# Optimization experiments

Measured on AMD Instinct MI355X. Metric: run time of the kernel, lower is better.

The kernel has to match this reference:

```python
import jax, jax.numpy as jnp
import numpy as np

N_EMBD = 384
HEAD_SIZE = 16

def setup_inputs() -> dict:
    key = jax.random.key(0)
    k1, k2, k3, k4 = jax.random.split(key, 4)
    B, T = 4, 4096
    x = jax.random.normal(k1, (B, T, N_EMBD), dtype=jnp.float32)
    # nn.Linear(n_embd, head_size, bias=False): y = x @ W^T, W: [head_size, n_embd].
    # Store transposed [n_embd, head_size] for direct matmul.
    s = 1.0 / np.sqrt(N_EMBD)
    Wk = jax.random.uniform(k2, (N_EMBD, HEAD_SIZE), jnp.float32, -s, s)
    Wq = jax.random.uniform(k3, (N_EMBD, HEAD_SIZE), jnp.float32, -s, s)
    Wv = jax.random.uniform(k4, (N_EMBD, HEAD_SIZE), jnp.float32, -s, s)
    return {"x": x, "Wk": Wk, "Wq": Wq, "Wv": Wv}

def reference(x, Wk, Wq, Wv):
    B, T, C = x.shape
    k = x @ Wk  # [B,T,H]
    q = x @ Wq
    v = x @ Wv
    scale = k.shape[-1] ** -0.5
    wei = jnp.einsum('bth,bsh->bts', q, k) * scale  # [B,T,T]
    causal = jnp.tril(jnp.ones((T, T), dtype=bool))
    wei = jnp.where(causal, wei, -jnp.inf)
    wei = jax.nn.softmax(wei, axis=-1)
    out = jnp.einsum('bts,bsh->bth', wei, v)  # [B,T,H]
    return out
```

## Files before the change

### kernel.cpp

```cpp
#include <hip/hip_runtime.h>


constexpr int B_DIM = 4;
constexpr int T_SEQ = 4096;
constexpr int C_DIM = 384;
constexpr int H_DIM = 16;
constexpr int NROW  = B_DIM * T_SEQ;
constexpr int NSLOT = 16;

typedef __bf16 bf16x8 __attribute__((ext_vector_type(8)));
typedef float  f32x4  __attribute__((ext_vector_type(4)));

__device__ __forceinline__ unsigned short f2bf(float f) {
  unsigned int u = __builtin_bit_cast(unsigned int, f);
  u += 0x7fffu + ((u >> 16) & 1u);
  return (unsigned short)(u >> 16);
}
__device__ __forceinline__ bf16x8 as_bf16x8(uint4 u) {
  return __builtin_bit_cast(bf16x8, u);
}
__device__ __forceinline__ unsigned cvt_pk_bf16(float lo, float hi) {
  unsigned r;
  asm("v_cvt_pk_bf16_f32 %0, %1, %2" : "=v"(r) : "v"(lo), "v"(hi));
  return r;
}

__global__ __launch_bounds__(256) void wconv(
    const float* __restrict__ Wk, const float* __restrict__ Wq,
    const float* __restrict__ Wv, unsigned short* __restrict__ WT) {
  const int i = blockIdx.x * 256 + threadIdx.x;
  const int m = i / 6144;
  const int r = i - m * 6144;
  const int n = r / 384;
  const int k = r - n * 384;
  const float* __restrict__ W = (m == 0) ? Wk : (m == 1) ? Wq : Wv;
  WT[i] = f2bf(W[k * 16 + n]);
}

__global__ __launch_bounds__(128) void qkv_mfma(
    const float* __restrict__ x, const unsigned short* __restrict__ WT,
    unsigned short* __restrict__ Kb,
    unsigned short* __restrict__ Qb,
    unsigned short* __restrict__ VTb)
{
  const int tid  = threadIdx.x;
  const int w    = tid >> 6;
  const int lane = tid & 63;
  const int quad = lane >> 4;
  const int col  = lane & 15;
  const int r0   = blockIdx.x << 4;
  const int kb   = w * 6;

  __shared__ float mrg[12][64];

  const float4* __restrict__ xp =
      reinterpret_cast<const float4*>(x + (size_t)(r0 + col) * C_DIM) + quad * 2;
  float4 araw[12];
#pragma unroll
  for (int kk = 0; kk < 6; ++kk) {
    araw[2 * kk]     = xp[(kb + kk) * 8];
    araw[2 * kk + 1] = xp[(kb + kk) * 8 + 1];
  }

  const uint4* __restrict__ bk = reinterpret_cast<const uint4*>(
      WT + (size_t)col * 384 + quad * 8);
  const uint4* __restrict__ bq = bk + 768;
  const uint4* __restrict__ bv = bk + 1536;

  f32x4 ck = {0.f, 0.f, 0.f, 0.f};
  f32x4 cq = {0.f, 0.f, 0.f, 0.f};
  f32x4 cv = {0.f, 0.f, 0.f, 0.f};
#pragma unroll
  for (int kk = 0; kk < 6; ++kk) {
    uint4 pk;
    const float4 a0 = araw[2 * kk], a1 = araw[2 * kk + 1];
    pk.x = cvt_pk_bf16(a0.x, a0.y);
    pk.y = cvt_pk_bf16(a0.z, a0.w);
    pk.z = cvt_pk_bf16(a1.x, a1.y);
    pk.w = cvt_pk_bf16(a1.z, a1.w);
    const bf16x8 av = as_bf16x8(pk);
    ck = __builtin_amdgcn_mfma_f32_16x16x32_bf16(av, as_bf16x8(bk[(kb + kk) * 4]), ck, 0, 0, 0);
    cq = __builtin_amdgcn_mfma_f32_16x16x32_bf16(av, as_bf16x8(bq[(kb + kk) * 4]), cq, 0, 0, 0);
    cv = __builtin_amdgcn_mfma_f32_16x16x32_bf16(av, as_bf16x8(bv[(kb + kk) * 4]), cv, 0, 0, 0);
  }

  if (w == 1) {
#pragma unroll
    for (int r = 0; r < 4; ++r) {
      mrg[r][lane]     = ck[r];
      mrg[4 + r][lane] = cq[r];
      mrg[8 + r][lane] = cv[r];
    }
  }
  __syncthreads();
  if (w == 0) {
    const float SC = 0.25f * 1.44269504088896341f;
#pragma unroll
    for (int r = 0; r < 4; ++r) {
      const float vk = ck[r] + mrg[r][lane];
      const float vq = cq[r] + mrg[4 + r][lane];
      const float vv = cv[r] + mrg[8 + r][lane];
      const int row = r0 + quad * 4 + r;
      Kb[row * 16 + col]      = f2bf(vk);
      Qb[row * 32 + col]      = f2bf(vq * SC);
      Qb[row * 32 + 16 + col] = 0;
      const int bb = row >> 12, t = row & 4095;
      VTb[(((size_t)(bb * 16 + col)) << 12) + t] = f2bf(vv);
    }
  }
}

__global__ __launch_bounds__(256, 8) void flash_v6(
    const unsigned short* __restrict__ Qb,
    const unsigned short* __restrict__ Kb,
    const unsigned short* __restrict__ VTb,
    float* __restrict__ PO, float* __restrict__ PL)
{
  const int tid  = threadIdx.x;
  const int w    = tid >> 6;
  const int lane = tid & 63;
  const int quad = lane >> 4;
  const int col  = lane & 15;
  const int p    = blockIdx.x >> 4;
  const int b    = (blockIdx.x >> 2) & 3;
  const int j    = blockIdx.x & 3;
  const int slot = (j << 2) | w;
  const int qtA  = 255 - p;
  const int qtB  = p;
  const int nchA = (qtA + 4) >> 2;

  __shared__ __attribute__((aligned(16))) unsigned short Pl[4][2][16 * 72];
  unsigned short* const Pb0 = Pl[w][0];

  const unsigned short* Kbase = Kb + ((size_t)(b * T_SEQ) << 4);
  const unsigned short* Vbase = VTb + (((size_t)(b * 16 + col)) << 12);
  const int poff = col * 72 + quad * 4;

  f32x4 o = {0.f, 0.f, 0.f, 0.f};

  auto buf = [&](int i) -> unsigned short* { return Pb0 + i * (16 * 72); };

  auto computeP = [&](int qt, bf16x8 qa, int c, unsigned short* P, float& lref) {
    const int kt0 = c << 2;
    f32x4 sf[4];
#pragma unroll
    for (int t = 0; t < 4; ++t) {
      const int kt = kt0 + t;
      if (kt <= qt) {
        const uint4* kp = reinterpret_cast<const uint4*>(
            Kbase + (((size_t)(kt * 16 + col)) << 4) + quad * 8);
        f32x4 z = {0.f, 0.f, 0.f, 0.f};
        sf[t] = __builtin_amdgcn_mfma_f32_16x16x32_bf16(as_bf16x8(kp[0]), qa, z, 0, 0, 0);
        if (kt == qt) {
#pragma unroll
          for (int r = 0; r < 4; ++r)
            if (quad * 4 + r > col) sf[t][r] = -1e30f;
        }
      } else {
#pragma unroll
        for (int r = 0; r < 4; ++r) sf[t][r] = -1e30f;
      }
    }
    float lsum = 0.f;
#pragma unroll
    for (int t = 0; t < 4; ++t) {
      const float p0 = __builtin_amdgcn_exp2f(sf[t][0]);
      const float p1 = __builtin_amdgcn_exp2f(sf[t][1]);
      const float p2 = __builtin_amdgcn_exp2f(sf[t][2]);
      const float p3 = __builtin_amdgcn_exp2f(sf[t][3]);
      lsum += (p0 + p1) + (p2 + p3);
      uint2 pr;
      pr.x = cvt_pk_bf16(p0, p1);
      pr.y = cvt_pk_bf16(p2, p3);
      *reinterpret_cast<uint2*>(P + poff + t * 16) = pr;
    }
    lref += lsum;
  };

  auto doPV = [&](int c, const unsigned short* P) {
    const uint4 v0 = *reinterpret_cast<const uint4*>(Vbase + c * 64 + quad * 8);
    const uint4 v1 = *reinterpret_cast<const uint4*>(Vbase + c * 64 + 32 + quad * 8);
    const uint4 p0 = *reinterpret_cast<const uint4*>(P + col * 72 + quad * 8);
    const uint4 p1 = *reinterpret_cast<const uint4*>(P + col * 72 + 32 + quad * 8);
    o = __builtin_amdgcn_mfma_f32_16x16x32_bf16(as_bf16x8(p0), as_bf16x8(v0), o, 0, 0, 0);
    o = __builtin_amdgcn_mfma_f32_16x16x32_bf16(as_bf16x8(p1), as_bf16x8(v1), o, 0, 0, 0);
  };

  auto writePartial = [&](int qt, float lsum) {
    float l = lsum;
    l += __shfl_xor(l, 16);
    l += __shfl_xor(l, 32);
    const size_t rowbase = (size_t)b * T_SEQ + ((size_t)qt << 4);
    float* pO = PO + ((size_t)slot * NROW + rowbase) * 16;
#pragma unroll
    for (int r = 0; r < 4; ++r)
      pO[(quad * 4 + r) * 16 + col] = o[r];
    if (quad == 0) PL[(size_t)slot * NROW + rowbase + col] = l;
  };

  const uint4* qpA = reinterpret_cast<const uint4*>(
      Qb + (((size_t)(b * T_SEQ + (qtA << 4) + col)) << 5) + quad * 8);
  const bf16x8 qaA = as_bf16x8(qpA[0]);

  float lA = 0.f, lB = 0.f;
  int g = slot;
  computeP(qtA, qaA, g, buf(0), lA);
  int prevC = g;
  int pb = 0;
  for (g += 16; g < nchA; g += 16) {
    computeP(qtA, qaA, g, buf(pb ^ 1), lA);
    doPV(prevC, buf(pb));
    prevC = g;
    pb ^= 1;
  }

  const int gB = g;
  bf16x8 qaB = qaA;
  if (gB < 65) {
    const uint4* qpB = reinterpret_cast<const uint4*>(
        Qb + (((size_t)(b * T_SEQ + (qtB << 4) + col)) << 5) + quad * 8);
    qaB = as_bf16x8(qpB[0]);
    computeP(qtB, qaB, gB - nchA, buf(pb ^ 1), lB);
  }
  doPV(prevC, buf(pb));
  writePartial(qtA, lA);
  o = (f32x4){0.f, 0.f, 0.f, 0.f};

  if (gB < 65) {
    pb ^= 1;
    int prevB = gB - nchA;
    for (int g2 = gB + 16; g2 < 65; g2 += 16) {
      computeP(qtB, qaB, g2 - nchA, buf(pb ^ 1), lB);
      doPV(prevB, buf(pb));
      prevB = g2 - nchA;
      pb ^= 1;
    }
    doPV(prevB, buf(pb));
  }
  writePartial(qtB, lB);
}

__global__ __launch_bounds__(256) void flash_merge(
    const float* __restrict__ PO, const float* __restrict__ PL,
    float* __restrict__ out)
{
  const int i   = blockIdx.x * 256 + threadIdx.x;
  const int row = i >> 4;
  float O = 0.f, L = 0.f;
#pragma unroll
  for (int s = 0; s < NSLOT; ++s) {
    O += PO[((size_t)s * NROW) * 16 + i];
    L += PL[(size_t)s * NROW + row];
  }
  out[i] = O / L;
}

extern "C" void kernel_launch(void* const* d_in, const int* in_sizes, int n_in,
                              void* d_out, int out_size, void* d_ws, size_t ws_size,
                              hipStream_t stream) {
  const float* x  = (const float*)d_in[0];
  const float* Wk = (const float*)d_in[1];
  const float* Wq = (const float*)d_in[2];
  const float* Wv = (const float*)d_in[3];
  float* outp = (float*)d_out;

  unsigned short* Qb  = (unsigned short*)d_ws;
  unsigned short* Kb  = Qb + (size_t)NROW * 32;
  unsigned short* VTb = Kb + (size_t)NROW * 16 + 64;
  unsigned short* WT  = VTb + (size_t)NROW * 16;
  float* PO = (float*)(WT + 18432);
  float* PL = PO + (size_t)NSLOT * NROW * 16;

  wconv<<<72, 256, 0, stream>>>(Wk, Wq, Wv, WT);
  qkv_mfma<<<1024, 128, 0, stream>>>(x, WT, Kb, Qb, VTb);
  flash_v6<<<2048, 256, 0, stream>>>(Qb, Kb, VTb, PO, PL);
  flash_merge<<<1024, 256, 0, stream>>>(PO, PL, outp);
}
```

Before: 104.5 us.

## Software-pipeline K/V global loads into registers, single P buffer in LDS

Restructures the flash kernel's main loop so K and V tiles for the next chunk are loaded into registers ahead of use, overlapping global-memory latency with the PV MFMA of the current chunk. The double-buffered P tile in shared memory is replaced by a single buffer, both query tiles are preloaded up front, and the A/B query phases are merged into one loop. It also drops the occupancy hint from launch bounds. This adds register pressure from the held K/V values, and relies on program order within a wavefront for the single P buffer to stay correct.

```diff
diff --git a/kernel.cpp b/kernel.cpp
--- a/kernel.cpp
+++ b/kernel.cpp
@@ -110,7 +110,7 @@
   }
 }
 
-__global__ __launch_bounds__(256, 8) void flash_v6(
+__global__ __launch_bounds__(256) void flash_v8(
     const unsigned short* __restrict__ Qb,
     const unsigned short* __restrict__ Kb,
     const unsigned short* __restrict__ VTb,
@@ -129,8 +129,8 @@
   const int qtB  = p;
   const int nchA = (qtA + 4) >> 2;
 
-  __shared__ __attribute__((aligned(16))) unsigned short Pl[4][2][16 * 72];
-  unsigned short* const Pb0 = Pl[w][0];
+  __shared__ __attribute__((aligned(16))) unsigned short Pl[4][16 * 72];
+  unsigned short* const P = Pl[w];
 
   const unsigned short* Kbase = Kb + ((size_t)(b * T_SEQ) << 4);
   const unsigned short* Vbase = VTb + (((size_t)(b * 16 + col)) << 12);
@@ -138,36 +138,48 @@
 
   f32x4 o = {0.f, 0.f, 0.f, 0.f};
 
-  auto buf = [&](int i) -> unsigned short* { return Pb0 + i * (16 * 72); };
-
-  auto computeP = [&](int qt, bf16x8 qa, int c, unsigned short* P, float& lref) {
+  const uint4* qpA = reinterpret_cast<const uint4*>(
+      Qb + (((size_t)(b * T_SEQ + (qtA << 4) + col)) << 5) + quad * 8);
+  const uint4* qpB = reinterpret_cast<const uint4*>(
+      Qb + (((size_t)(b * T_SEQ + (qtB << 4) + col)) << 5) + quad * 8);
+  const bf16x8 qaA = as_bf16x8(qpA[0]);
+  const bf16x8 qaB = as_bf16x8(qpB[0]);
+
+  auto loadK = [&](int c, uint4* k4) {
     const int kt0 = c << 2;
-    f32x4 sf[4];
+#pragma unroll
+    for (int t = 0; t < 4; ++t)
+      k4[t] = *reinterpret_cast<const uint4*>(
+          Kbase + (((size_t)((kt0 + t) * 16 + col)) << 4) + quad * 8);
+  };
+  auto loadV = [&](int c, uint4* v2) {
+    v2[0] = *reinterpret_cast<const uint4*>(Vbase + c * 64 + quad * 8);
+    v2[1] = *reinterpret_cast<const uint4*>(Vbase + c * 64 + 32 + quad * 8);
+  };
+
+  auto computeP = [&](int qt, bf16x8 qa, int c, const uint4* k4, float& lref) {
+    const int kt0 = c << 2;
+    float lsum = 0.f;
 #pragma unroll
     for (int t = 0; t < 4; ++t) {
       const int kt = kt0 + t;
+      f32x4 sf;
       if (kt <= qt) {
-        const uint4* kp = reinterpret_cast<const uint4*>(
-            Kbase + (((size_t)(kt * 16 + col)) << 4) + quad * 8);
         f32x4 z = {0.f, 0.f, 0.f, 0.f};
-        sf[t] = __builtin_amdgcn_mfma_f32_16x16x32_bf16(as_bf16x8(kp[0]), qa, z, 0, 0, 0);
+        sf = __builtin_amdgcn_mfma_f32_16x16x32_bf16(as_bf16x8(k4[t]), qa, z, 0, 0, 0);
         if (kt == qt) {
 #pragma unroll
           for (int r = 0; r < 4; ++r)
-            if (quad * 4 + r > col) sf[t][r] = -1e30f;
+            if (quad * 4 + r > col) sf[r] = -1e30f;
         }
       } else {
 #pragma unroll
-        for (int r = 0; r < 4; ++r) sf[t][r] = -1e30f;
+        for (int r = 0; r < 4; ++r) sf[r] = -1e30f;
       }
-    }
-    float lsum = 0.f;
-#pragma unroll
-    for (int t = 0; t < 4; ++t) {
-      const float p0 = __builtin_amdgcn_exp2f(sf[t][0]);
-      const float p1 = __builtin_amdgcn_exp2f(sf[t][1]);
-      const float p2 = __builtin_amdgcn_exp2f(sf[t][2]);
-      const float p3 = __builtin_amdgcn_exp2f(sf[t][3]);
+      const float p0 = __builtin_amdgcn_exp2f(sf[0]);
+      const float p1 = __builtin_amdgcn_exp2f(sf[1]);
+      const float p2 = __builtin_amdgcn_exp2f(sf[2]);
+      const float p3 = __builtin_amdgcn_exp2f(sf[3]);
       lsum += (p0 + p1) + (p2 + p3);
       uint2 pr;
       pr.x = cvt_pk_bf16(p0, p1);
@@ -177,13 +189,14 @@
     lref += lsum;
   };
 
-  auto doPV = [&](int c, const unsigned short* P) {
-    const uint4 v0 = *reinterpret_cast<const uint4*>(Vbase + c * 64 + quad * 8);
-    const uint4 v1 = *reinterpret_cast<const uint4*>(Vbase + c * 64 + 32 + quad * 8);
-    const uint4 p0 = *reinterpret_cast<const uint4*>(P + col * 72 + quad * 8);
-    const uint4 p1 = *reinterpret_cast<const uint4*>(P + col * 72 + 32 + quad * 8);
-    o = __builtin_amdgcn_mfma_f32_16x16x32_bf16(as_bf16x8(p0), as_bf16x8(v0), o, 0, 0, 0);
-    o = __builtin_amdgcn_mfma_f32_16x16x32_bf16(as_bf16x8(p1), as_bf16x8(v1), o, 0, 0, 0);
+  auto doPV = [&](const uint4* v2) {
+    const uint2* pp = reinterpret_cast<const uint2*>(P + col * 72);
+    const uint2 a0 = pp[quad * 2],     a1 = pp[quad * 2 + 1];
+    const uint2 b0 = pp[8 + quad * 2], b1 = pp[8 + quad * 2 + 1];
+    const uint4 p0 = {a0.x, a0.y, a1.x, a1.y};
+    const uint4 p1 = {b0.x, b0.y, b1.x, b1.y};
+    o = __builtin_amdgcn_mfma_f32_16x16x32_bf16(as_bf16x8(p0), as_bf16x8(v2[0]), o, 0, 0, 0);
+    o = __builtin_amdgcn_mfma_f32_16x16x32_bf16(as_bf16x8(p1), as_bf16x8(v2[1]), o, 0, 0, 0);
   };
 
   auto writePartial = [&](int qt, float lsum) {
@@ -198,46 +211,41 @@
     if (quad == 0) PL[(size_t)slot * NROW + rowbase + col] = l;
   };
 
-  const uint4* qpA = reinterpret_cast<const uint4*>(
-      Qb + (((size_t)(b * T_SEQ + (qtA << 4) + col)) << 5) + quad * 8);
-  const bf16x8 qaA = as_bf16x8(qpA[0]);
-
   float lA = 0.f, lB = 0.f;
+  uint4 k4[4], vcur[2], vnxt[2];
+
   int g = slot;
-  computeP(qtA, qaA, g, buf(0), lA);
-  int prevC = g;
-  int pb = 0;
-  for (g += 16; g < nchA; g += 16) {
-    computeP(qtA, qaA, g, buf(pb ^ 1), lA);
-    doPV(prevC, buf(pb));
-    prevC = g;
-    pb ^= 1;
-  }
-
-  const int gB = g;
-  bf16x8 qaB = qaA;
-  if (gB < 65) {
-    const uint4* qpB = reinterpret_cast<const uint4*>(
-        Qb + (((size_t)(b * T_SEQ + (qtB << 4) + col)) << 5) + quad * 8);
-    qaB = as_bf16x8(qpB[0]);
-    computeP(qtB, qaB, gB - nchA, buf(pb ^ 1), lB);
-  }
-  doPV(prevC, buf(pb));
-  writePartial(qtA, lA);
-  o = (f32x4){0.f, 0.f, 0.f, 0.f};
-
-  if (gB < 65) {
-    pb ^= 1;
-    int prevB = gB - nchA;
-    for (int g2 = gB + 16; g2 < 65; g2 += 16) {
-      computeP(qtB, qaB, g2 - nchA, buf(pb ^ 1), lB);
-      doPV(prevB, buf(pb));
-      prevB = g2 - nchA;
-      pb ^= 1;
-    }
-    doPV(prevB, buf(pb));
-  }
-  writePartial(qtB, lB);
+  loadK(g, k4);
+  loadV(g, vcur);
+  computeP(qtA, qaA, g, k4, lA);
+
+  int prevg = g;
+  g += 16;
+  while (g < 65) {
+    const int c = (g < nchA) ? g : g - nchA;
+    loadK(c, k4);
+    loadV(c, vnxt);
+    doPV(vcur);
+    asm volatile("" ::: "memory");
+    if (prevg < nchA && g >= nchA) {
+      writePartial(qtA, lA);
+      o = (f32x4){0.f, 0.f, 0.f, 0.f};
+    }
+    if (g < nchA) computeP(qtA, qaA, c, k4, lA);
+    else          computeP(qtB, qaB, c, k4, lB);
+    vcur[0] = vnxt[0];
+    vcur[1] = vnxt[1];
+    prevg = g;
+    g += 16;
+  }
+  doPV(vcur);
+  if (prevg < nchA) {
+    writePartial(qtA, lA);
+    o = (f32x4){0.f, 0.f, 0.f, 0.f};
+    writePartial(qtB, 0.f);
+  } else {
+    writePartial(qtB, lB);
+  }
 }
 
 __global__ __launch_bounds__(256) void flash_merge(
@@ -273,6 +281,6 @@
 
   wconv<<<72, 256, 0, stream>>>(Wk, Wq, Wv, WT);
   qkv_mfma<<<1024, 128, 0, stream>>>(x, WT, Kb, Qb, VTb);
-  flash_v6<<<2048, 256, 0, stream>>>(Qb, Kb, VTb, PO, PL);
+  flash_v8<<<2048, 256, 0, stream>>>(Qb, Kb, VTb, PO, PL);
   flash_merge<<<1024, 256, 0, stream>>>(PO, PL, outp);
 }
```

After: 102.7 us. About the same (-1.7%).
